# Kernel tuning notes

Hardware: AMD Instinct MI355X
Metric: run time of the kernel (lower is better)

Reference implementation:

```python
import jax, jax.numpy as jnp
import numpy as np

B = 4
NUM_S = 512                 # sampled centers per layer -> S = 8*NUM_S = 4096 neighbor pairs
TAU = 0.01                  # forward() default tau passed to PatchNCELoss
LAYERS = [(64, 256, 256), (128, 128, 128), (256, 64, 64), (512, 32, 32)]  # (C,H,W) VGG-style


def _make_ids(h, w, num_s, rng):
    # Faithful to NeighborSample: random interior centers + their 8-neighborhood.
    perm = rng.permutation((h - 2) * (w - 2))[:num_s]
    ch = perm // (w - 2) + 1
    cw = perm % (w - 2) + 1
    c = ch * w + cw
    c_ids = np.tile(c, 8)
    delta = np.repeat(np.array([-(w + 1), -w, -(w - 1), -1, 1, w - 1, w, w + 1]), num_s)
    return c_ids.astype(np.int32), (c_ids + delta).astype(np.int32)


def setup_inputs() -> dict:
    key = jax.random.key(0)
    rng = np.random.default_rng(0)
    keys = iter(jax.random.split(key, 64))
    inp = {}
    for i, (c, h, w) in enumerate(LAYERS):
        inp[f'fq{i}'] = jax.random.normal(next(keys), (B, c, h, w), jnp.float32)
        inp[f'fk{i}'] = jax.random.normal(next(keys), (B, c, h, w), jnp.float32)
        cid, nid = _make_ids(h, w, NUM_S, rng)
        inp[f'cid{i}'] = jnp.asarray(cid)
        inp[f'nid{i}'] = jnp.asarray(nid)
        for j, (din, dout) in enumerate([(c, c), (c, c), (c, c // 4)]):
            scale = np.float32(1.0 / np.sqrt(din))
            inp[f'w{i}_{j}'] = jax.random.normal(next(keys), (dout, din), jnp.float32) * scale
            inp[f'b{i}_{j}'] = jnp.zeros((dout,), jnp.float32)
    return inp


def _sample(feat, cid, nid, Ws, bs):
    # NeighborSample: gather center/neighbor features, difference, 3-Linear MLP.
    b, c, h, w = feat.shape
    fr = feat.transpose(0, 2, 3, 1).reshape(b, h * w, c)   # [B, HW, C]
    d = fr[:, cid] - fr[:, nid]                            # [B, S, C]
    d = jax.nn.relu(d @ Ws[0].T + bs[0])
    d = jax.nn.relu(d @ Ws[1].T + bs[1])
    d = d @ Ws[2].T + bs[2]                                # [B, S, Cout]
    return jnp.transpose(d, (0, 2, 1))                     # [B, Cout, S] (Normalize is identity)


def _patch_nce(f_q, f_k, tau):
    f_k = jax.lax.stop_gradient(f_k)                       # f_k.detach()
    l_pos = jnp.sum(f_q * f_k, axis=1)[:, :, None]         # [B, S, 1]
    l_neg = jnp.einsum('bcs,bct->bst', f_q, f_k)           # [B, S, S]
    s = f_q.shape[2]
    l_neg = jnp.where(jnp.eye(s, dtype=bool), -jnp.inf, l_neg)
    logits = jnp.concatenate([l_pos, l_neg], axis=2) / tau # [B, S, S+1]
    # CE with target class 0 == -mean log_softmax[..., 0]
    return -jnp.mean(jax.nn.log_softmax(logits, axis=-1)[..., 0])


def _ccpl(args):
    loss = jnp.float32(0.0)
    for i in range(4):
        Ws = [args[f'w{i}_{j}'] for j in range(3)]
        bs = [args[f'b{i}_{j}'] for j in range(3)]
        f_q = _sample(args[f'fq{i}'], args[f'cid{i}'], args[f'nid{i}'], Ws, bs)
        f_k = _sample(args[f'fk{i}'], args[f'cid{i}'], args[f'nid{i}'], Ws, bs)
        loss = loss + _patch_nce(f_q, f_k, TAU)
    return loss


def reference(fq0, fk0, cid0, nid0, w0_0, b0_0, w0_1, b0_1, w0_2, b0_2,
              fq1, fk1, cid1, nid1, w1_0, b1_0, w1_1, b1_1, w1_2, b1_2,
              fq2, fk2, cid2, nid2, w2_0, b2_0, w2_1, b2_1, w2_2, b2_2,
              fq3, fk3, cid3, nid3, w3_0, b3_0, w3_1, b3_1, w3_2, b3_2):
    return _ccpl(dict(locals()))
```

## Files before the change

kernel.cpp:

```cpp
#include <hip/hip_runtime.h>
#include <hip/hip_bf16.h>
#include <math.h>

#define S_TOTAL 4096
#define B_TOTAL 4
#define M_TOTAL 16384
#define M2_TOTAL 32768
#define NSLICE 8

typedef __attribute__((ext_vector_type(8))) short bf16x8;
typedef __attribute__((ext_vector_type(4))) float f32x4;

__device__ __forceinline__ void glds16(const void* src, void* lds_base) {
    __builtin_amdgcn_global_load_lds(
        (const __attribute__((address_space(1))) void*)src,
        (__attribute__((address_space(3))) void*)lds_base, 16, 0, 0);
}

__device__ __forceinline__ int swz(int cg, int row, int GR) {
    return (GR == 4) ? (cg ^ ((row >> 1) & 3)) : (cg ^ (row & 7));
}

struct WArgs { const float* s[12]; __hip_bfloat16* d[12]; int n[12]; };
__global__ __launch_bounds__(256) void convert_w(WArgs a) {
    int mtx = blockIdx.y, n = a.n[mtx];
    const float* s = a.s[mtx];
    __hip_bfloat16* d = a.d[mtx];
    for (int i = blockIdx.x * 256 + threadIdx.x; i < n; i += gridDim.x * 256)
        d[i] = __float2bfloat16(s[i]);
}

template<int BN>
__global__ __launch_bounds__(256) void gemm_map(
    const float* __restrict__ feat,
    const __hip_bfloat16* __restrict__ W,
    __hip_bfloat16* __restrict__ U,
    int K, int HW)
{
    constexpr int WN = (BN == 128) ? 2 : 1;
    constexpr int WM = 4 / WN;
    constexpr int RM = 128 / WM, RN = BN / WN;
    constexpr int TMI = RM / 16, TNI = RN / 16;
    __shared__ __hip_bfloat16 Bs[BN * 32];
    const int lane = threadIdx.x & 63, wave = threadIdx.x >> 6;
    const int quad = lane >> 4, l15 = lane & 15;
    const int wm = wave % WM, wn = wave / WM;
    const int m0 = blockIdx.y * 128, n0 = blockIdx.x * BN;
    const int b = blockIdx.z;
    const float* Ab = feat + (size_t)b * K * HW;

    f32x4 acc[TMI][TNI];
#pragma unroll
    for (int i = 0; i < TMI; ++i)
#pragma unroll
        for (int j = 0; j < TNI; ++j) acc[i][j] = (f32x4){0.f, 0.f, 0.f, 0.f};

    for (int k0 = 0; k0 < K; k0 += 32) {
        for (int g0 = wave * 64; g0 < BN * 4; g0 += 256) {
            int g = g0 + lane, row = g >> 2, cg = g & 3;
            glds16(W + (size_t)(n0 + row) * K + k0 + swz(cg, row, 4) * 8,
                   (char*)Bs + g0 * 16);
        }
        __syncthreads();
        bf16x8 af[TMI];
#pragma unroll
        for (int i = 0; i < TMI; ++i) {
            const float* ap = Ab + (size_t)(k0 + quad * 8) * HW
                            + (m0 + wm * RM + i * 16 + l15);
#pragma unroll
            for (int j = 0; j < 8; ++j) {
                __hip_bfloat16 h = __float2bfloat16(ap[(size_t)j * HW]);
                af[i][j] = *(short*)&h;
            }
        }
        bf16x8 bfr[TNI];
#pragma unroll
        for (int j = 0; j < TNI; ++j) {
            int row = wn * RN + j * 16 + l15;
            bfr[j] = *(const bf16x8*)(Bs + row * 32 + swz(quad, row, 4) * 8);
        }
#pragma unroll
        for (int i = 0; i < TMI; ++i)
#pragma unroll
            for (int j = 0; j < TNI; ++j)
                acc[i][j] = __builtin_amdgcn_mfma_f32_16x16x32_bf16(
                    af[i], bfr[j], acc[i][j], 0, 0, 0);
        __syncthreads();
    }
#pragma unroll
    for (int j = 0; j < TNI; ++j) {
        int col = n0 + wn * RN + j * 16 + l15;
#pragma unroll
        for (int i = 0; i < TMI; ++i) {
            int row = m0 + wm * RM + i * 16 + quad * 4;
#pragma unroll
            for (int r = 0; r < 4; ++r)
                U[((size_t)b * HW + row + r) * K + col] = __float2bfloat16(acc[i][j][r]);
        }
    }
}

__global__ __launch_bounds__(256) void gather2(
    const __hip_bfloat16* __restrict__ U, const int* __restrict__ cid,
    const int* __restrict__ nid, const float* __restrict__ b0,
    __hip_bfloat16* __restrict__ X, int C, int HW, int z)
{
    int wv = threadIdx.x >> 6, lane = threadIdx.x & 63;
    int r = blockIdx.x * 4 + wv;
    int s = r & 4095, b = r >> 12;
    int ci = cid[s], ni = nid[s];
    const __hip_bfloat16* up = U + ((size_t)b * HW + ci) * C;
    const __hip_bfloat16* un = U + ((size_t)b * HW + ni) * C;
    __hip_bfloat16* xo = X + ((size_t)z * M_TOTAL + r) * C;
    for (int c = lane; c < C; c += 64) {
        float v = __bfloat162float(up[c]) - __bfloat162float(un[c]) + b0[c];
        xo[c] = __float2bfloat16(fmaxf(v, 0.f));
    }
}

template<int BN>
__global__ __launch_bounds__(256) void gemm_mfma(
    const __hip_bfloat16* __restrict__ X, const __hip_bfloat16* __restrict__ W,
    const float* __restrict__ bias, __hip_bfloat16* __restrict__ Y,
    int K, int ldY, int relu)
{
    constexpr int WN = (BN == 128) ? 2 : 1;
    constexpr int WM = 4 / WN;
    constexpr int RM = 128 / WM, RN = BN / WN;
    constexpr int TMI = RM / 16, TNI = RN / 16;
    __shared__ __hip_bfloat16 As[128 * 32];
    __shared__ __hip_bfloat16 Bs[BN * 32];
    const int lane = threadIdx.x & 63, wave = threadIdx.x >> 6;
    const int quad = lane >> 4, l15 = lane & 15;
    const int wm = wave % WM, wn = wave / WM;
    const int m0 = blockIdx.y * 128, n0 = blockIdx.x * BN;

    f32x4 acc[TMI][TNI];
#pragma unroll
    for (int i = 0; i < TMI; ++i)
#pragma unroll
        for (int j = 0; j < TNI; ++j) acc[i][j] = (f32x4){0.f, 0.f, 0.f, 0.f};

    for (int k0 = 0; k0 < K; k0 += 32) {
        for (int h = 0; h < 2; ++h) {
            int g0 = h * 256 + wave * 64;
            int g = g0 + lane, row = g >> 2, cg = g & 3;
            glds16(X + (size_t)(m0 + row) * K + k0 + swz(cg, row, 4) * 8,
                   (char*)As + g0 * 16);
        }
        for (int g0 = wave * 64; g0 < BN * 4; g0 += 256) {
            int g = g0 + lane, row = g >> 2, cg = g & 3;
            glds16(W + (size_t)(n0 + row) * K + k0 + swz(cg, row, 4) * 8,
                   (char*)Bs + g0 * 16);
        }
        __syncthreads();
        bf16x8 af[TMI], bfr[TNI];
#pragma unroll
        for (int i = 0; i < TMI; ++i) {
            int row = wm * RM + i * 16 + l15;
            af[i] = *(const bf16x8*)(As + row * 32 + swz(quad, row, 4) * 8);
        }
#pragma unroll
        for (int j = 0; j < TNI; ++j) {
            int row = wn * RN + j * 16 + l15;
            bfr[j] = *(const bf16x8*)(Bs + row * 32 + swz(quad, row, 4) * 8);
        }
#pragma unroll
        for (int i = 0; i < TMI; ++i)
#pragma unroll
            for (int j = 0; j < TNI; ++j)
                acc[i][j] = __builtin_amdgcn_mfma_f32_16x16x32_bf16(
                    af[i], bfr[j], acc[i][j], 0, 0, 0);
        __syncthreads();
    }

#pragma unroll
    for (int j = 0; j < TNI; ++j) {
        int col = n0 + wn * RN + j * 16 + l15;
        float bv = bias[col];
#pragma unroll
        for (int i = 0; i < TMI; ++i) {
            int row = m0 + wm * RM + i * 16 + quad * 4;
#pragma unroll
            for (int r = 0; r < 4; ++r) {
                float v = acc[i][j][r] + bv;
                if (relu) v = fmaxf(v, 0.f);
                Y[(size_t)(row + r) * ldY + col] = __float2bfloat16(v);
            }
        }
    }
}

template<int KPAD>
__device__ __forceinline__ void nce_stage(
    const __hip_bfloat16* __restrict__ Kb, __hip_bfloat16* KsBuf, int wave, int lane)
{
    constexpr int GR = KPAD / 8;
    for (int g0 = wave * 64; g0 < 128 * GR; g0 += 256) {
        int g = g0 + lane, row = g / GR, cg = g % GR;
        glds16(Kb + (size_t)row * KPAD + swz(cg, row, GR) * 8,
               (char*)KsBuf + g0 * 16);
    }
}

template<int KPAD, int TI, int MINW>
__global__ __launch_bounds__(256, MINW) void nce_mfma(
    const __hip_bfloat16* __restrict__ Fq, const __hip_bfloat16* __restrict__ Fk,
    float2* __restrict__ partial, float s2)
{
    constexpr int KS = KPAD / 32;
    constexpr int GR = KPAD / 8;
    constexpr int QT = TI * 64;
    constexpr int BLK_X = S_TOTAL / QT;
    constexpr int TILE = 128 * KPAD;
    __shared__ __hip_bfloat16 Ks[2 * TILE];
    const int lane = threadIdx.x & 63, wave = threadIdx.x >> 6;
    const int quad = lane >> 4, l15 = lane & 15;

    constexpr int NWG = BLK_X * NSLICE * B_TOTAL;
    int lid = blockIdx.x + BLK_X * (blockIdx.y + NSLICE * blockIdx.z);
    int sid = (lid & 7) * (NWG / 8) + (lid >> 3);
    const int r0 = (sid % BLK_X) * QT;
    const int slice = (sid / BLK_X) % NSLICE;
    const int bb = sid / (BLK_X * NSLICE);

    bf16x8 qf[TI][KS];
    const __hip_bfloat16* Qb = Fq + ((size_t)bb * S_TOTAL + r0 + wave * TI * 16) * KPAD;
#pragma unroll
    for (int i = 0; i < TI; ++i)
#pragma unroll
        for (int s = 0; s < KS; ++s)
            qf[i][s] = *(const bf16x8*)(Qb + (size_t)(i * 16 + l15) * KPAD + s * 32 + quad * 8);

    float m[TI * 4], l[TI * 4];
#pragma unroll
    for (int i = 0; i < TI * 4; ++i) { m[i] = -1e30f; l[i] = 0.f; }

    const int t_begin = slice * (S_TOTAL / NSLICE);
    const int t_end = t_begin + S_TOTAL / NSLICE;
    const __hip_bfloat16* KbBase = Fk + (size_t)bb * S_TOTAL * KPAD;

    nce_stage<KPAD>(KbBase + (size_t)t_begin * KPAD, Ks, wave, lane);
    __syncthreads();
    int cur = 0;
    for (int t0 = t_begin; t0 < t_end; t0 += 128) {
        if (t0 + 128 < t_end)
            nce_stage<KPAD>(KbBase + (size_t)(t0 + 128) * KPAD, Ks + (cur ^ 1) * TILE, wave, lane);

        f32x4 acc[TI][8];
#pragma unroll
        for (int i = 0; i < TI; ++i)
#pragma unroll
            for (int j = 0; j < 8; ++j) acc[i][j] = (f32x4){0.f, 0.f, 0.f, 0.f};

        const __hip_bfloat16* Kc = Ks + cur * TILE;
#pragma unroll
        for (int s = 0; s < KS; ++s) {
            bf16x8 bfr[8];
#pragma unroll
            for (int j = 0; j < 8; ++j) {
                int row = j * 16 + l15;
                bfr[j] = *(const bf16x8*)(Kc + (size_t)row * KPAD + swz(s * 4 + quad, row, GR) * 8);
            }
#pragma unroll
            for (int i = 0; i < TI; ++i)
#pragma unroll
                for (int j = 0; j < 8; ++j)
                    acc[i][j] = __builtin_amdgcn_mfma_f32_16x16x32_bf16(
                        qf[i][s], bfr[j], acc[i][j], 0, 0, 0);
        }

#pragma unroll
        for (int i = 0; i < TI; ++i)
#pragma unroll
            for (int r = 0; r < 4; ++r) {
                int idx = i * 4 + r;
                float vmax = acc[i][0][r];
#pragma unroll
                for (int j = 1; j < 8; ++j) vmax = fmaxf(vmax, acc[i][j][r]);
                float mn = fmaxf(m[idx], vmax);
                float ms = mn * s2;
                float lv = l[idx] * exp2f(fmaf(m[idx], s2, -ms));
#pragma unroll
                for (int j = 0; j < 8; ++j)
                    lv += exp2f(fmaf(acc[i][j][r], s2, -ms));
                m[idx] = mn; l[idx] = lv;
            }
        __syncthreads();
        cur ^= 1;
    }

#pragma unroll
    for (int off = 1; off < 16; off <<= 1)
#pragma unroll
        for (int i = 0; i < TI * 4; ++i) {
            float mo = __shfl_xor(m[i], off);
            float lo = __shfl_xor(l[i], off);
            float mn = fmaxf(m[i], mo);
            l[i] = l[i] * exp2f((m[i] - mn) * s2) + lo * exp2f((mo - mn) * s2);
            m[i] = mn;
        }
    if (l15 == 0) {
        size_t base = (size_t)(bb * NSLICE + slice) * S_TOTAL;
#pragma unroll
        for (int i = 0; i < TI; ++i)
#pragma unroll
            for (int r = 0; r < 4; ++r) {
                int row = r0 + wave * TI * 16 + i * 16 + quad * 4 + r;
                partial[base + row] = make_float2(m[i * 4 + r], l[i * 4 + r]);
            }
    }
}

__global__ __launch_bounds__(256) void nce_reduce(
    const __hip_bfloat16* __restrict__ Fq, const __hip_bfloat16* __restrict__ Fk,
    const float2* __restrict__ partial, float* __restrict__ out,
    int KPAD, float s2, float inv_tau)
{
    __shared__ float red[4];
    const int tid = threadIdx.x;
    const int g = blockIdx.x * 256 + tid;
    const int bb = g >> 12, s = g & 4095;

    float M = -1e30f, L = 0.f;
    for (int p = 0; p < NSLICE; ++p) {
        float2 pr = partial[(size_t)(bb * NSLICE + p) * S_TOTAL + s];
        float mn = fmaxf(M, pr.x);
        L = L * exp2f((M - mn) * s2) + pr.y * exp2f((pr.x - mn) * s2);
        M = mn;
    }
    const __hip_bfloat16* q = Fq + (size_t)g * KPAD;
    const __hip_bfloat16* k = Fk + (size_t)g * KPAD;
    float pos = 0.f;
    for (int c = 0; c < KPAD; c += 8) {
        bf16x8 a = *(const bf16x8*)(q + c);
        bf16x8 b = *(const bf16x8*)(k + c);
#pragma unroll
        for (int j = 0; j < 8; ++j) {
            __hip_bfloat16 ha, hb;
            *(short*)&ha = a[j]; *(short*)&hb = b[j];
            pos += __bfloat162float(ha) * __bfloat162float(hb);
        }
    }
    float v = 0.6931471805599453f * (M * s2 + log2f(L)) - pos * inv_tau;
#pragma unroll
    for (int off = 1; off < 64; off <<= 1) v += __shfl_xor(v, off);
    if ((tid & 63) == 0) red[tid >> 6] = v;
    __syncthreads();
    if (tid == 0)
        atomicAdd(out, (red[0] + red[1] + red[2] + red[3]) * (1.0f / (float)M_TOTAL));
}

static void launch_gemm(const __hip_bfloat16* X, const __hip_bfloat16* W,
                        const float* bias, __hip_bfloat16* Y,
                        int N, int K, int ldY, int relu, hipStream_t st)
{
    const int gy = M2_TOTAL / 128;
    if (N >= 128)
        gemm_mfma<128><<<dim3(N / 128, gy), 256, 0, st>>>(X, W, bias, Y, K, ldY, relu);
    else if (N == 64)
        gemm_mfma<64><<<dim3(1, gy), 256, 0, st>>>(X, W, bias, Y, K, ldY, relu);
    else if (N == 32)
        gemm_mfma<32><<<dim3(1, gy), 256, 0, st>>>(X, W, bias, Y, K, ldY, relu);
    else
        gemm_mfma<16><<<dim3(1, gy), 256, 0, st>>>(X, W, bias, Y, K, ldY, relu);
}

static void launch_map(const float* feat, const __hip_bfloat16* W0,
                       __hip_bfloat16* U, int C, int HW, hipStream_t st)
{
    if (C >= 128)
        gemm_map<128><<<dim3(C / 128, HW / 128, B_TOTAL), 256, 0, st>>>(feat, W0, U, C, HW);
    else
        gemm_map<64><<<dim3(1, HW / 128, B_TOTAL), 256, 0, st>>>(feat, W0, U, C, HW);
}

extern "C" void kernel_launch(void* const* d_in, const int* in_sizes, int n_in,
                              void* d_out, int out_size, void* d_ws, size_t ws_size,
                              hipStream_t stream)
{
    (void)in_sizes; (void)n_in; (void)out_size; (void)ws_size;
    hipMemsetAsync(d_out, 0, sizeof(float), stream);

    static const int Cs[4]  = {64, 128, 256, 512};
    static const int HWs[4] = {256 * 256, 128 * 128, 64 * 64, 32 * 32};
    const float s2 = 144.26950408889634f;

    char* p = (char*)d_ws;
    char* region1 = p;                       p += (size_t)32 * 1024 * 1024;
    __hip_bfloat16* Xb = (__hip_bfloat16*)p; p += (size_t)M2_TOTAL * 512 * 2;
    __hip_bfloat16* F  = (__hip_bfloat16*)p; p += (size_t)M2_TOTAL * 128 * 2;
    __hip_bfloat16* wb = (__hip_bfloat16*)p;
    __hip_bfloat16* U  = (__hip_bfloat16*)region1;
    __hip_bfloat16* Yb = (__hip_bfloat16*)region1;
    float2* partial    = (float2*)region1;

    WArgs wa;
    size_t off = 0;
    for (int i = 0; i < 4; ++i)
        for (int j = 0; j < 3; ++j) {
            int N = (j == 2) ? Cs[i] / 4 : Cs[i];
            int K = Cs[i];
            wa.s[i * 3 + j] = (const float*)d_in[i * 10 + 4 + j * 2];
            wa.d[i * 3 + j] = wb + off;
            wa.n[i * 3 + j] = N * K;
            off += (size_t)N * K;
        }
    convert_w<<<dim3(64, 12), 256, 0, stream>>>(wa);

    for (int i = 0; i < 4; ++i) {
        const int C = Cs[i], HW = HWs[i], Cout = C / 4;
        const int Kpad = (Cout < 32) ? 32 : Cout;
        const float* fq  = (const float*)d_in[i * 10 + 0];
        const float* fk  = (const float*)d_in[i * 10 + 1];
        const int*   cid = (const int*)  d_in[i * 10 + 2];
        const int*   nid = (const int*)  d_in[i * 10 + 3];
        const float* b0  = (const float*)d_in[i * 10 + 5];
        const float* b1  = (const float*)d_in[i * 10 + 7];
        const float* b2  = (const float*)d_in[i * 10 + 9];

        if (Kpad > Cout)
            hipMemsetAsync(F, 0, (size_t)M2_TOTAL * Kpad * 2, stream);

        for (int z = 0; z < 2; ++z) {
            launch_map(z ? fk : fq, wa.d[i * 3 + 0], U, C, HW, stream);
            gather2<<<dim3(M_TOTAL / 4), 256, 0, stream>>>(
                U, cid, nid, b0, Xb, C, HW, z);
        }
        launch_gemm(Xb, wa.d[i * 3 + 1], b1, Yb, C, C, C, 1, stream);
        launch_gemm(Yb, wa.d[i * 3 + 2], b2, F, Cout, C, Kpad, 0, stream);

        const __hip_bfloat16* Fq = F;
        const __hip_bfloat16* Fk = F + (size_t)M_TOTAL * Kpad;
        if (Kpad == 32) {
            dim3 ngrid(S_TOTAL / 256, NSLICE, B_TOTAL);
            nce_mfma<32, 4, 2><<<ngrid, 256, 0, stream>>>(Fq, Fk, partial, s2);
        } else if (Kpad == 64) {
            dim3 ngrid(S_TOTAL / 256, NSLICE, B_TOTAL);
            nce_mfma<64, 4, 2><<<ngrid, 256, 0, stream>>>(Fq, Fk, partial, s2);
        } else {
            dim3 ngrid(S_TOTAL / 128, NSLICE, B_TOTAL);
            nce_mfma<128, 2, 2><<<ngrid, 256, 0, stream>>>(Fq, Fk, partial, s2);
        }

        nce_reduce<<<dim3(M_TOTAL / 256), 256, 0, stream>>>(
            Fq, Fk, partial, (float*)d_out, Kpad, s2, 100.0f);
    }
}
```

Baseline: 692.0 us.

## Gather-diff first GEMM for layer 0, deepen NCE K-tile prefetch, retune tiles

For layer 0 (C=64, HW=65536), the code now gathers center-minus-neighbor differences straight from the fp32 NCHW features and runs the first linear layer as a GEMM on 32768 rows. Before, it mapped all 65536 pixels through the first layer and gathered afterwards, so the new path removes work over pixels that are never sampled, at the cost of strided gathers along C. The NCE kernel now prefetches two tiles ahead with explicit vmcnt waits and raw barriers, raises wave priority around the MFMA loop, and reduces the max as a tree. All Kpad variants now use TI=2, which doubles the NCE grid for the small-K layers, and the swizzle is extended for GR=16.

```diff
diff --git a/kernel.cpp b/kernel.cpp
--- a/kernel.cpp
+++ b/kernel.cpp
@@ -18,7 +18,9 @@
 }
 
 __device__ __forceinline__ int swz(int cg, int row, int GR) {
-    return (GR == 4) ? (cg ^ ((row >> 1) & 3)) : (cg ^ (row & 7));
+    if (GR == 4) return cg ^ ((row >> 1) & 3);
+    if (GR == 8) return cg ^ (row & 7);
+    return cg ^ (row & 15);
 }
 
 struct WArgs { const float* s[12]; __hip_bfloat16* d[12]; int n[12]; };
@@ -118,6 +120,24 @@
     }
 }
 
+__global__ __launch_bounds__(256) void gatherdiff(
+    const float* __restrict__ fq, const float* __restrict__ fk,
+    const int* __restrict__ cid, const int* __restrict__ nid,
+    __hip_bfloat16* __restrict__ D, int C, int HW)
+{
+    int wv = threadIdx.x >> 6, lane = threadIdx.x & 63;
+    int r = blockIdx.x * 4 + wv;
+    int z = r >> 14, rr = r & 16383;
+    int s = rr & 4095, b = rr >> 12;
+    int ci = cid[s], ni = nid[s];
+    const float* f = (z ? fk : fq) + (size_t)b * C * HW;
+    __hip_bfloat16* xo = D + (size_t)r * C;
+    for (int c = lane; c < C; c += 64) {
+        float v = f[(size_t)c * HW + ci] - f[(size_t)c * HW + ni];
+        xo[c] = __float2bfloat16(v);
+    }
+}
+
 template<int BN>
 __global__ __launch_bounds__(256) void gemm_mfma(
     const __hip_bfloat16* __restrict__ X, const __hip_bfloat16* __restrict__ W,
@@ -196,6 +216,7 @@
     const __hip_bfloat16* __restrict__ Kb, __hip_bfloat16* KsBuf, int wave, int lane)
 {
     constexpr int GR = KPAD / 8;
+#pragma unroll
     for (int g0 = wave * 64; g0 < 128 * GR; g0 += 256) {
         int g = g0 + lane, row = g / GR, cg = g % GR;
         glds16(Kb + (size_t)row * KPAD + swz(cg, row, GR) * 8,
@@ -213,6 +234,8 @@
     constexpr int QT = TI * 64;
     constexpr int BLK_X = S_TOTAL / QT;
     constexpr int TILE = 128 * KPAD;
+    constexpr int LPS = (128 * GR) / 256;
+    constexpr int NT = (S_TOTAL / NSLICE) / 128;
     __shared__ __hip_bfloat16 Ks[2 * TILE];
     const int lane = threadIdx.x & 63, wave = threadIdx.x >> 6;
     const int quad = lane >> 4, l15 = lane & 15;
@@ -237,15 +260,18 @@
     for (int i = 0; i < TI * 4; ++i) { m[i] = -1e30f; l[i] = 0.f; }
 
     const int t_begin = slice * (S_TOTAL / NSLICE);
-    const int t_end = t_begin + S_TOTAL / NSLICE;
-    const __hip_bfloat16* KbBase = Fk + (size_t)bb * S_TOTAL * KPAD;
-
-    nce_stage<KPAD>(KbBase + (size_t)t_begin * KPAD, Ks, wave, lane);
-    __syncthreads();
-    int cur = 0;
-    for (int t0 = t_begin; t0 < t_end; t0 += 128) {
-        if (t0 + 128 < t_end)
-            nce_stage<KPAD>(KbBase + (size_t)(t0 + 128) * KPAD, Ks + (cur ^ 1) * TILE, wave, lane);
+    const __hip_bfloat16* Kt = Fk + ((size_t)bb * S_TOTAL + t_begin) * KPAD;
+
+    nce_stage<KPAD>(Kt, Ks, wave, lane);
+    nce_stage<KPAD>(Kt + (size_t)128 * KPAD, Ks + TILE, wave, lane);
+
+#pragma unroll
+    for (int t = 0; t < NT; ++t) {
+        if (t + 1 < NT)
+            asm volatile("s_waitcnt vmcnt(%0)" :: "i"(LPS) : "memory");
+        else
+            asm volatile("s_waitcnt vmcnt(0)" ::: "memory");
+        __builtin_amdgcn_s_barrier();
 
         f32x4 acc[TI][8];
 #pragma unroll
@@ -253,7 +279,8 @@
 #pragma unroll
             for (int j = 0; j < 8; ++j) acc[i][j] = (f32x4){0.f, 0.f, 0.f, 0.f};
 
-        const __hip_bfloat16* Kc = Ks + cur * TILE;
+        const __hip_bfloat16* Kc = Ks + (t & 1) * TILE;
+        __builtin_amdgcn_s_setprio(1);
 #pragma unroll
         for (int s = 0; s < KS; ++s) {
             bf16x8 bfr[8];
@@ -269,15 +296,18 @@
                     acc[i][j] = __builtin_amdgcn_mfma_f32_16x16x32_bf16(
                         qf[i][s], bfr[j], acc[i][j], 0, 0, 0);
         }
+        __builtin_amdgcn_s_setprio(0);
 
 #pragma unroll
         for (int i = 0; i < TI; ++i)
 #pragma unroll
             for (int r = 0; r < 4; ++r) {
                 int idx = i * 4 + r;
-                float vmax = acc[i][0][r];
-#pragma unroll
-                for (int j = 1; j < 8; ++j) vmax = fmaxf(vmax, acc[i][j][r]);
+                float v01 = fmaxf(acc[i][0][r], acc[i][1][r]);
+                float v23 = fmaxf(acc[i][2][r], acc[i][3][r]);
+                float v45 = fmaxf(acc[i][4][r], acc[i][5][r]);
+                float v67 = fmaxf(acc[i][6][r], acc[i][7][r]);
+                float vmax = fmaxf(fmaxf(v01, v23), fmaxf(v45, v67));
                 float mn = fmaxf(m[idx], vmax);
                 float ms = mn * s2;
                 float lv = l[idx] * exp2f(fmaf(m[idx], s2, -ms));
@@ -286,8 +316,10 @@
                     lv += exp2f(fmaf(acc[i][j][r], s2, -ms));
                 m[idx] = mn; l[idx] = lv;
             }
-        __syncthreads();
-        cur ^= 1;
+        __builtin_amdgcn_s_barrier();
+        if (t + 2 < NT)
+            nce_stage<KPAD>(Kt + (size_t)(t + 2) * 128 * KPAD,
+                            Ks + (t & 1) * TILE, wave, lane);
     }
 
 #pragma unroll
@@ -422,26 +454,30 @@
         if (Kpad > Cout)
             hipMemsetAsync(F, 0, (size_t)M2_TOTAL * Kpad * 2, stream);
 
-        for (int z = 0; z < 2; ++z) {
-            launch_map(z ? fk : fq, wa.d[i * 3 + 0], U, C, HW, stream);
-            gather2<<<dim3(M_TOTAL / 4), 256, 0, stream>>>(
-                U, cid, nid, b0, Xb, C, HW, z);
+        if (i == 0) {
+            __hip_bfloat16* D = U;
+            gatherdiff<<<dim3(M2_TOTAL / 4), 256, 0, stream>>>(
+                fq, fk, cid, nid, D, C, HW);
+            launch_gemm(D, wa.d[i * 3 + 0], b0, Xb, C, C, C, 1, stream);
+        } else {
+            for (int z = 0; z < 2; ++z) {
+                launch_map(z ? fk : fq, wa.d[i * 3 + 0], U, C, HW, stream);
+                gather2<<<dim3(M_TOTAL / 4), 256, 0, stream>>>(
+                    U, cid, nid, b0, Xb, C, HW, z);
+            }
         }
         launch_gemm(Xb, wa.d[i * 3 + 1], b1, Yb, C, C, C, 1, stream);
         launch_gemm(Yb, wa.d[i * 3 + 2], b2, F, Cout, C, Kpad, 0, stream);
 
         const __hip_bfloat16* Fq = F;
         const __hip_bfloat16* Fk = F + (size_t)M_TOTAL * Kpad;
-        if (Kpad == 32) {
-            dim3 ngrid(S_TOTAL / 256, NSLICE, B_TOTAL);
-            nce_mfma<32, 4, 2><<<ngrid, 256, 0, stream>>>(Fq, Fk, partial, s2);
-        } else if (Kpad == 64) {
-            dim3 ngrid(S_TOTAL / 256, NSLICE, B_TOTAL);
-            nce_mfma<64, 4, 2><<<ngrid, 256, 0, stream>>>(Fq, Fk, partial, s2);
-        } else {
-            dim3 ngrid(S_TOTAL / 128, NSLICE, B_TOTAL);
+        dim3 ngrid(S_TOTAL / 128, NSLICE, B_TOTAL);
+        if (Kpad == 32)
+            nce_mfma<32, 2, 2><<<ngrid, 256, 0, stream>>>(Fq, Fk, partial, s2);
+        else if (Kpad == 64)
+            nce_mfma<64, 2, 2><<<ngrid, 256, 0, stream>>>(Fq, Fk, partial, s2);
+        else
             nce_mfma<128, 2, 2><<<ngrid, 256, 0, stream>>>(Fq, Fk, partial, s2);
-        }
 
         nce_reduce<<<dim3(M_TOTAL / 256), 256, 0, stream>>>(
             Fq, Fk, partial, (float*)d_out, Kpad, s2, 100.0f);
```

Measured after the change: 656.8 us. 5.1% less time.
